# Optimization experiments

Hardware: AMD Instinct MI355X
Metric: run time of the kernel (lower is better)

## Reference

```python
import jax, jax.numpy as jnp
import numpy as np

N_TOKENS = 32768
DIM = 2048
N_EXPERTS = 64
TOP_K = 8
N_GROUP = 8
TOPK_GROUP = 4
ROUTE_SCALE = 2.5
EPS = 1e-20


def setup_inputs() -> dict:
    key = jax.random.key(0)
    k1, k2 = jax.random.split(key)
    hidden_states = jax.random.normal(k1, (N_TOKENS, DIM), dtype=jnp.float32)
    weight = jax.random.normal(k2, (N_EXPERTS, DIM), dtype=jnp.float32) * 0.02
    e_score_correction_bias = jnp.zeros((N_EXPERTS,), dtype=jnp.float32)
    return {"hidden_states": hidden_states, "weight": weight,
            "e_score_correction_bias": e_score_correction_bias}


def reference(hidden_states, weight, e_score_correction_bias):
    # router logits in fp32: [N, E]
    logits = jnp.einsum('nd,ed->ne', hidden_states.astype(jnp.float32),
                        weight.astype(jnp.float32))
    scores = jax.nn.sigmoid(logits)  # score_func == 'sigmoid'

    # --- top-k index selection (no-grad path in torch) ---
    sfc = scores + e_score_correction_bias[None, :]  # [N, E]
    per_group = N_EXPERTS // N_GROUP
    # group score = sum of top-2 scores within each group: [N, G]
    grouped = sfc.reshape(-1, N_GROUP, per_group)
    group_scores = jax.lax.top_k(grouped, 2)[0].sum(axis=-1)
    # pick top `TOPK_GROUP` groups
    _, group_idx = jax.lax.top_k(group_scores, TOPK_GROUP)  # [N, topk_group]
    n = group_scores.shape[0]
    group_mask = jnp.zeros_like(group_scores).at[
        jnp.arange(n)[:, None], group_idx].set(1.0)  # [N, G]
    score_mask = jnp.repeat(group_mask, per_group, axis=1)  # [N, E]
    masked_scores = jnp.where(score_mask > 0, sfc, 0.0)
    _, topk_indices = jax.lax.top_k(masked_scores, TOP_K)  # [N, top_k]

    # gather weights from *unbiased* scores, normalize, scale
    topk_weights = jnp.take_along_axis(scores, topk_indices, axis=1)
    denom = topk_weights.sum(axis=-1, keepdims=True) + EPS
    topk_weights = topk_weights / denom * ROUTE_SCALE
    return topk_indices, topk_weights
```

## Files before the change

### kernel.cpp

```cpp
#include <hip/hip_runtime.h>
#include <math.h>

#define NT 32768
#define DIM 2048
#define NE 64
#define RSCALE 2.5f
#define REPS 1e-20f
#define KC 64
#define NCHK (DIM / KC)
#define TOKB 32

#define WL_OFF 12288
#define BS_OFF 36864
#define ARENA 37120

typedef __attribute__((ext_vector_type(8))) short short8x;
typedef __attribute__((ext_vector_type(4))) float f32x4;
typedef __attribute__((ext_vector_type(4))) unsigned int uint4x;

#define PACKHI(odd, even) __builtin_amdgcn_perm((odd), (even), 0x07060302u)

__device__ __forceinline__ void decomp4(f32x4 x, unsigned int o[6]) {
    unsigned int u0 = __float_as_uint(x.x), u1 = __float_as_uint(x.y);
    unsigned int u2 = __float_as_uint(x.z), u3 = __float_as_uint(x.w);
    o[0] = PACKHI(u1, u0); o[1] = PACKHI(u3, u2);
    float r0 = x.x - __uint_as_float(u0 & 0xffff0000u);
    float r1 = x.y - __uint_as_float(u1 & 0xffff0000u);
    float r2 = x.z - __uint_as_float(u2 & 0xffff0000u);
    float r3 = x.w - __uint_as_float(u3 & 0xffff0000u);
    unsigned int v0 = __float_as_uint(r0), v1 = __float_as_uint(r1);
    unsigned int v2 = __float_as_uint(r2), v3 = __float_as_uint(r3);
    o[2] = PACKHI(v1, v0); o[3] = PACKHI(v3, v2);
    float s0 = r0 - __uint_as_float(v0 & 0xffff0000u);
    float s1 = r1 - __uint_as_float(v1 & 0xffff0000u);
    float s2 = r2 - __uint_as_float(v2 & 0xffff0000u);
    float s3 = r3 - __uint_as_float(v3 & 0xffff0000u);
    o[4] = PACKHI(__float_as_uint(s1), __float_as_uint(s0));
    o[5] = PACKHI(__float_as_uint(s3), __float_as_uint(s2));
}

__device__ __forceinline__ void decomp8(f32x4 a, f32x4 b,
                                        short8x* f0, short8x* f1, short8x* f2) {
    unsigned int oa[6], ob[6];
    decomp4(a, oa); decomp4(b, ob);
    uint4x t0 = {oa[0], oa[1], ob[0], ob[1]};
    uint4x t1 = {oa[2], oa[3], ob[2], ob[3]};
    uint4x t2 = {oa[4], oa[5], ob[4], ob[5]};
    *f0 = __builtin_bit_cast(short8x, t0);
    *f1 = __builtin_bit_cast(short8x, t1);
    *f2 = __builtin_bit_cast(short8x, t2);
}

#define BARRIER() do { \
    asm volatile("s_waitcnt lgkmcnt(0)" ::: "memory"); \
    __builtin_amdgcn_s_barrier(); \
    __builtin_amdgcn_sched_barrier(0); \
} while (0)

#define STAGE_ISSUE(H0, H1, W0, W1, W2, W3, KOFF) do { \
    H0 = *(const f32x4*)(hgsrc + (KOFF)); \
    H1 = *(const f32x4*)(hgsrc + (KOFF) + 4); \
    W0 = *(const f32x4*)(wgsrc + (KOFF)); \
    W1 = *(const f32x4*)(wgsrc + (KOFF) + 4); \
    W2 = *(const f32x4*)(wgsrc + (KOFF) + 8); \
    W3 = *(const f32x4*)(wgsrc + (KOFF) + 12); \
} while (0)

#define STAGE_WRITE(H0, H1, W0, W1, W2, W3) do { \
    short8x f0_, f1_, f2_; \
    decomp8(H0, H1, &f0_, &f1_, &f2_); \
    *(short8x*)(arena + 0    + hoff) = f0_; \
    *(short8x*)(arena + 4096 + hoff) = f1_; \
    *(short8x*)(arena + 8192 + hoff) = f2_; \
    decomp8(W0, W1, &f0_, &f1_, &f2_); \
    *(short8x*)(arena + WL_OFF + 0     + woff0) = f0_; \
    *(short8x*)(arena + WL_OFF + 8192  + woff0) = f1_; \
    *(short8x*)(arena + WL_OFF + 16384 + woff0) = f2_; \
    decomp8(W2, W3, &f0_, &f1_, &f2_); \
    *(short8x*)(arena + WL_OFF + 0     + woff1) = f0_; \
    *(short8x*)(arena + WL_OFF + 8192  + woff1) = f1_; \
    *(short8x*)(arena + WL_OFF + 16384 + woff1) = f2_; \
} while (0)

#define COMPUTE() do { \
    _Pragma("unroll") \
    for (int kk = 0; kk < 2; ++kk) { \
        short8x a0[2], a1[2], a2[2]; \
        _Pragma("unroll") \
        for (int tt = 0; tt < 2; ++tt) { \
            const int r_ = tt * 16 + l15; \
            const int sb = r_ * 128 + (((kk * 4 + g) ^ (r_ & 7)) << 4); \
            a0[tt] = *(const short8x*)(arena + 0    + sb); \
            a1[tt] = *(const short8x*)(arena + 4096 + sb); \
            a2[tt] = *(const short8x*)(arena + 8192 + sb); \
        } \
        const int rw = w * 16 + l15; \
        const int wb = rw * 128 + (((kk * 4 + g) ^ (rw & 7)) << 4); \
        short8x b0 = *(const short8x*)(arena + WL_OFF + 0     + wb); \
        short8x b1 = *(const short8x*)(arena + WL_OFF + 8192  + wb); \
        short8x b2 = *(const short8x*)(arena + WL_OFF + 16384 + wb); \
        _Pragma("unroll") \
        for (int tt = 0; tt < 2; ++tt) { \
            Cm[tt] = __builtin_amdgcn_mfma_f32_16x16x32_bf16(a0[tt], b0, Cm[tt], 0, 0, 0); \
            Cc[tt] = __builtin_amdgcn_mfma_f32_16x16x32_bf16(a1[tt], b0, Cc[tt], 0, 0, 0); \
            Cc[tt] = __builtin_amdgcn_mfma_f32_16x16x32_bf16(a2[tt], b0, Cc[tt], 0, 0, 0); \
            Cc[tt] = __builtin_amdgcn_mfma_f32_16x16x32_bf16(a0[tt], b1, Cc[tt], 0, 0, 0); \
            Cc[tt] = __builtin_amdgcn_mfma_f32_16x16x32_bf16(a1[tt], b1, Cc[tt], 0, 0, 0); \
            Cc[tt] = __builtin_amdgcn_mfma_f32_16x16x32_bf16(a0[tt], b2, Cc[tt], 0, 0, 0); \
        } \
    } \
} while (0)

#define DRAIN do { \
    _Pragma("unroll") \
    for (int tt = 0; tt < 2; ++tt) { \
        _Pragma("unroll") \
        for (int r = 0; r < 4; ++r) \
            md[tt][r] += (double)Cm[tt][r] + (double)Cc[tt][r]; \
        Cm[tt] = (f32x4)0.0f; Cc[tt] = (f32x4)0.0f; \
    } \
} while (0)

__global__ __launch_bounds__(256, 4) void router_kernel(
    const float* __restrict__ H,
    const float* __restrict__ W,
    const float* __restrict__ B,
    float* __restrict__ out)
{
    __shared__ __align__(16) char arena[ARENA];
    float* bsf = (float*)(arena + BS_OFF);
    float* scf = (float*)(arena);

    const int tid  = threadIdx.x;
    const int lane = tid & 63;
    const int w    = __builtin_amdgcn_readfirstlane(tid >> 6);
    const int l15  = lane & 15, g = lane >> 4;
    const size_t tb = (size_t)blockIdx.x * TOKB;

    if (tid < NE) bsf[tid] = B[tid];

    const int hrow = tid >> 3, hq = tid & 7;
    const int wrow = tid >> 2, wq = (tid & 3) << 1;
    const float* hgsrc = H + (tb + (size_t)hrow) * DIM + hq * 8;
    const float* wgsrc = W + (size_t)wrow * DIM + wq * 8;
    const int hoff  = hrow * 128 + ((hq ^ (hrow & 7)) << 4);
    const int woff0 = wrow * 128 + ((wq ^ (wrow & 7)) << 4);
    const int woff1 = wrow * 128 + (((wq + 1) ^ (wrow & 7)) << 4);

    f32x4 Cm[2], Cc[2];
    double md[2][4];
    #pragma unroll
    for (int tt = 0; tt < 2; ++tt) {
        Cm[tt] = (f32x4)0.0f; Cc[tt] = (f32x4)0.0f;
        #pragma unroll
        for (int r = 0; r < 4; ++r) md[tt][r] = 0.0;
    }

    f32x4 hA0, hA1, wA0, wA1, wA2, wA3;
    f32x4 hB0, hB1, wB0, wB1, wB2, wB3;

    STAGE_ISSUE(hA0, hA1, wA0, wA1, wA2, wA3, 0);
    STAGE_ISSUE(hB0, hB1, wB0, wB1, wB2, wB3, KC);
    STAGE_WRITE(hA0, hA1, wA0, wA1, wA2, wA3);
    BARRIER();

    for (int chb = 0; chb < NCHK; chb += 2) {
        COMPUTE();
        if (chb + 2 < NCHK) STAGE_ISSUE(hA0, hA1, wA0, wA1, wA2, wA3, (chb + 2) * KC);
        BARRIER();
        STAGE_WRITE(hB0, hB1, wB0, wB1, wB2, wB3);
        BARRIER();

        COMPUTE();
        if (chb + 3 < NCHK) STAGE_ISSUE(hB0, hB1, wB0, wB1, wB2, wB3, (chb + 3) * KC);
        if (((chb + 1) & 3) == 3) DRAIN;
        BARRIER();
        if (chb + 2 < NCHK) STAGE_WRITE(hA0, hA1, wA0, wA1, wA2, wA3);
        BARRIER();
    }

    #pragma unroll
    for (int tt = 0; tt < 2; ++tt)
        #pragma unroll
        for (int r = 0; r < 4; ++r) {
            float logit = (float)md[tt][r];
            float s = 1.0f / (1.0f + expf(-logit));
            int t = tt * 16 + g * 4 + r;
            int e = w * 16 + l15;
            scf[t * 65 + e] = s;
        }
    __syncthreads();

    if ((tid & 7) == 0) {
        const int t = tid >> 3;
        const float* sc = &scf[t * 65];
        float gs[8];
        #pragma unroll
        for (int gg = 0; gg < 8; ++gg) {
            float m1 = -1e30f, m2 = -1e30f;
            #pragma unroll
            for (int j = 0; j < 8; ++j) {
                float v = sc[gg * 8 + j] + bsf[gg * 8 + j];
                if (v > m1) { m2 = m1; m1 = v; }
                else if (v > m2) { m2 = v; }
            }
            gs[gg] = m1 + m2;
        }
        unsigned gmask = 0;
        for (int i = 0; i < 4; ++i) {
            float best = -1e30f; int bg = 0;
            for (int gg = 0; gg < 8; ++gg)
                if (!((gmask >> gg) & 1u) && gs[gg] > best) { best = gs[gg]; bg = gg; }
            gmask |= 1u << bg;
        }
        unsigned long long picked = 0ull;
        int   idxs[8];
        float wts[8];
        float wsum = 0.0f;
        for (int i = 0; i < 8; ++i) {
            float best = -1e30f; int bi = 0;
            for (int e = 0; e < 64; ++e) {
                if ((picked >> e) & 1ull) continue;
                float v = ((gmask >> (e >> 3)) & 1u) ? (sc[e] + bsf[e]) : 0.0f;
                if (v > best) { best = v; bi = e; }
            }
            picked |= 1ull << bi;
            idxs[i] = bi;
            wts[i] = sc[bi];
            wsum += sc[bi];
        }
        const float scale = RSCALE / (wsum + REPS);
        const size_t token = tb + t;
        #pragma unroll
        for (int i = 0; i < 8; ++i) {
            out[token * 8 + i] = (float)idxs[i];
            out[(size_t)NT * 8 + token * 8 + i] = wts[i] * scale;
        }
    }
}

extern "C" void kernel_launch(void* const* d_in, const int* in_sizes, int n_in,
                              void* d_out, int out_size, void* d_ws, size_t ws_size,
                              hipStream_t stream) {
    (void)in_sizes; (void)n_in; (void)out_size; (void)d_ws; (void)ws_size;
    const float* H = (const float*)d_in[0];
    const float* W = (const float*)d_in[1];
    const float* B = (const float*)d_in[2];
    float* out = (float*)d_out;
    router_kernel<<<dim3(NT / TOKB), dim3(256), 0, stream>>>(H, W, B, out);
}
```

Baseline: 148.9 us.

## Pre-split weights once and stream per-wave slices via direct global-to-LDS loads

Adds a small prep kernel that splits the router weight into three bf16 parts in a pre-swizzled global image. The main kernel then loads each wave's weight slice straight into a per-wave LDS region with global_load_lds, and keeps hidden-state chunks in registers, splitting them right before the MFMAs. This removes the block-wide barriers, the per-block weight split work and the LDS staging of activations, and it halves the K chunk size. The costs are an extra kernel launch, a hand-set vmcnt wait that must stay in step with the number of loads in flight, and redundant hidden loads, since every wave reads all 32 token rows.

New measurement: 221.3 us. +48.6%, slower.

```diff
diff --git a/kernel.cpp b/kernel.cpp
--- a/kernel.cpp
+++ b/kernel.cpp
@@ -6,17 +6,22 @@
 #define NE 64
 #define RSCALE 2.5f
 #define REPS 1e-20f
-#define KC 64
-#define NCHK (DIM / KC)
+#define KC 32
+#define NCH (DIM / KC)
 #define TOKB 32
 
-#define WL_OFF 12288
-#define BS_OFF 36864
-#define ARENA 37120
-
+#define WAVE_LDS 6144
+#define BUF_STRIDE 3072
+#define BS_OFF 24576
+#define ARENA 24832
+
+typedef const __attribute__((address_space(1))) void GV;
+typedef __attribute__((address_space(3))) void LV;
 typedef __attribute__((ext_vector_type(8))) short short8x;
 typedef __attribute__((ext_vector_type(4))) float f32x4;
 typedef __attribute__((ext_vector_type(4))) unsigned int uint4x;
+
+__device__ __align__(16) char WImg[NCH][3 * 4096];
 
 #define PACKHI(odd, even) __builtin_amdgcn_perm((odd), (even), 0x07060302u)
 
@@ -51,63 +56,59 @@
     *f2 = __builtin_bit_cast(short8x, t2);
 }
 
-#define BARRIER() do { \
-    asm volatile("s_waitcnt lgkmcnt(0)" ::: "memory"); \
-    __builtin_amdgcn_s_barrier(); \
-    __builtin_amdgcn_sched_barrier(0); \
-} while (0)
-
-#define STAGE_ISSUE(H0, H1, W0, W1, W2, W3, KOFF) do { \
-    H0 = *(const f32x4*)(hgsrc + (KOFF)); \
-    H1 = *(const f32x4*)(hgsrc + (KOFF) + 4); \
-    W0 = *(const f32x4*)(wgsrc + (KOFF)); \
-    W1 = *(const f32x4*)(wgsrc + (KOFF) + 4); \
-    W2 = *(const f32x4*)(wgsrc + (KOFF) + 8); \
-    W3 = *(const f32x4*)(wgsrc + (KOFF) + 12); \
-} while (0)
-
-#define STAGE_WRITE(H0, H1, W0, W1, W2, W3) do { \
-    short8x f0_, f1_, f2_; \
-    decomp8(H0, H1, &f0_, &f1_, &f2_); \
-    *(short8x*)(arena + 0    + hoff) = f0_; \
-    *(short8x*)(arena + 4096 + hoff) = f1_; \
-    *(short8x*)(arena + 8192 + hoff) = f2_; \
-    decomp8(W0, W1, &f0_, &f1_, &f2_); \
-    *(short8x*)(arena + WL_OFF + 0     + woff0) = f0_; \
-    *(short8x*)(arena + WL_OFF + 8192  + woff0) = f1_; \
-    *(short8x*)(arena + WL_OFF + 16384 + woff0) = f2_; \
-    decomp8(W2, W3, &f0_, &f1_, &f2_); \
-    *(short8x*)(arena + WL_OFF + 0     + woff1) = f0_; \
-    *(short8x*)(arena + WL_OFF + 8192  + woff1) = f1_; \
-    *(short8x*)(arena + WL_OFF + 16384 + woff1) = f2_; \
-} while (0)
-
-#define COMPUTE() do { \
+__global__ void prep_w_kernel(const float* __restrict__ W) {
+    const int ch = blockIdx.x;
+    const int tid = threadIdx.x;
+    const int srow = tid >> 2;
+    const int sq   = tid & 3;
+    const float* src = W + (size_t)srow * DIM + ch * KC + sq * 8;
+    f32x4 lo = *(const f32x4*)src;
+    f32x4 hi = *(const f32x4*)(src + 4);
+    short8x f0, f1, f2;
+    decomp8(lo, hi, &f0, &f1, &f2);
+    const int soff = srow * 64 + ((sq ^ ((srow >> 1) & 3)) << 4);
+    *(short8x*)&WImg[ch][0 * 4096 + soff] = f0;
+    *(short8x*)&WImg[ch][1 * 4096 + soff] = f1;
+    *(short8x*)&WImg[ch][2 * 4096 + soff] = f2;
+}
+
+#define SB __builtin_amdgcn_sched_barrier(0)
+
+#define VWAIT() do { SB; asm volatile("s_waitcnt vmcnt(7)" ::: "memory"); SB; } while (0)
+
+#define HSTAGE(R0, R1, R2, R3, CHN) do { \
+    const float* p0_ = hg0 + (CHN) * KC; \
+    const float* p1_ = hg1 + (CHN) * KC; \
+    R0 = *(const f32x4*)p0_; R1 = *(const f32x4*)(p0_ + 4); \
+    R2 = *(const f32x4*)p1_; R3 = *(const f32x4*)(p1_ + 4); \
+} while (0)
+
+#define WSTAGE(CHN, BUFB) do { \
+    const char* ws_ = WImg[(CHN)]; \
+    __builtin_amdgcn_global_load_lds((GV*)(ws_ + 0 * 4096 + wimg_off), \
+        (LV*)(warena + (BUFB) + 0 * 1024), 16, 0, 0); \
+    __builtin_amdgcn_global_load_lds((GV*)(ws_ + 1 * 4096 + wimg_off), \
+        (LV*)(warena + (BUFB) + 1 * 1024), 16, 0, 0); \
+    __builtin_amdgcn_global_load_lds((GV*)(ws_ + 2 * 4096 + wimg_off), \
+        (LV*)(warena + (BUFB) + 2 * 1024), 16, 0, 0); \
+} while (0)
+
+#define COMPUTE(BUFB, R0, R1, R2, R3) do { \
+    short8x a0[2], a1[2], a2[2]; \
+    decomp8(R0, R1, &a0[0], &a1[0], &a2[0]); \
+    decomp8(R2, R3, &a0[1], &a1[1], &a2[1]); \
+    const char* wb_ = warena + (BUFB); \
+    short8x b0 = *(const short8x*)(wb_ + 0 * 1024 + bo); \
+    short8x b1 = *(const short8x*)(wb_ + 1 * 1024 + bo); \
+    short8x b2 = *(const short8x*)(wb_ + 2 * 1024 + bo); \
     _Pragma("unroll") \
-    for (int kk = 0; kk < 2; ++kk) { \
-        short8x a0[2], a1[2], a2[2]; \
-        _Pragma("unroll") \
-        for (int tt = 0; tt < 2; ++tt) { \
-            const int r_ = tt * 16 + l15; \
-            const int sb = r_ * 128 + (((kk * 4 + g) ^ (r_ & 7)) << 4); \
-            a0[tt] = *(const short8x*)(arena + 0    + sb); \
-            a1[tt] = *(const short8x*)(arena + 4096 + sb); \
-            a2[tt] = *(const short8x*)(arena + 8192 + sb); \
-        } \
-        const int rw = w * 16 + l15; \
-        const int wb = rw * 128 + (((kk * 4 + g) ^ (rw & 7)) << 4); \
-        short8x b0 = *(const short8x*)(arena + WL_OFF + 0     + wb); \
-        short8x b1 = *(const short8x*)(arena + WL_OFF + 8192  + wb); \
-        short8x b2 = *(const short8x*)(arena + WL_OFF + 16384 + wb); \
-        _Pragma("unroll") \
-        for (int tt = 0; tt < 2; ++tt) { \
-            Cm[tt] = __builtin_amdgcn_mfma_f32_16x16x32_bf16(a0[tt], b0, Cm[tt], 0, 0, 0); \
-            Cc[tt] = __builtin_amdgcn_mfma_f32_16x16x32_bf16(a1[tt], b0, Cc[tt], 0, 0, 0); \
-            Cc[tt] = __builtin_amdgcn_mfma_f32_16x16x32_bf16(a2[tt], b0, Cc[tt], 0, 0, 0); \
-            Cc[tt] = __builtin_amdgcn_mfma_f32_16x16x32_bf16(a0[tt], b1, Cc[tt], 0, 0, 0); \
-            Cc[tt] = __builtin_amdgcn_mfma_f32_16x16x32_bf16(a1[tt], b1, Cc[tt], 0, 0, 0); \
-            Cc[tt] = __builtin_amdgcn_mfma_f32_16x16x32_bf16(a0[tt], b2, Cc[tt], 0, 0, 0); \
-        } \
+    for (int tt = 0; tt < 2; ++tt) { \
+        Cm[tt] = __builtin_amdgcn_mfma_f32_16x16x32_bf16(a0[tt], b0, Cm[tt], 0, 0, 0); \
+        Cc[tt] = __builtin_amdgcn_mfma_f32_16x16x32_bf16(a1[tt], b0, Cc[tt], 0, 0, 0); \
+        Cc[tt] = __builtin_amdgcn_mfma_f32_16x16x32_bf16(a2[tt], b0, Cc[tt], 0, 0, 0); \
+        Cc[tt] = __builtin_amdgcn_mfma_f32_16x16x32_bf16(a0[tt], b1, Cc[tt], 0, 0, 0); \
+        Cc[tt] = __builtin_amdgcn_mfma_f32_16x16x32_bf16(a1[tt], b1, Cc[tt], 0, 0, 0); \
+        Cc[tt] = __builtin_amdgcn_mfma_f32_16x16x32_bf16(a0[tt], b2, Cc[tt], 0, 0, 0); \
     } \
 } while (0)
 
@@ -123,7 +124,6 @@
 
 __global__ __launch_bounds__(256, 4) void router_kernel(
     const float* __restrict__ H,
-    const float* __restrict__ W,
     const float* __restrict__ B,
     float* __restrict__ out)
 {
@@ -137,15 +137,13 @@
     const int l15  = lane & 15, g = lane >> 4;
     const size_t tb = (size_t)blockIdx.x * TOKB;
 
-    if (tid < NE) bsf[tid] = B[tid];
-
-    const int hrow = tid >> 3, hq = tid & 7;
-    const int wrow = tid >> 2, wq = (tid & 3) << 1;
-    const float* hgsrc = H + (tb + (size_t)hrow) * DIM + hq * 8;
-    const float* wgsrc = W + (size_t)wrow * DIM + wq * 8;
-    const int hoff  = hrow * 128 + ((hq ^ (hrow & 7)) << 4);
-    const int woff0 = wrow * 128 + ((wq ^ (wrow & 7)) << 4);
-    const int woff1 = wrow * 128 + (((wq + 1) ^ (wrow & 7)) << 4);
+    float breg = (tid < NE) ? B[tid] : 0.0f;
+
+    char* warena = arena + w * WAVE_LDS;
+    const int wimg_off = w * 1024 + lane * 16;
+    const float* hg0 = H + (tb + (size_t)l15) * DIM + g * 8;
+    const float* hg1 = H + (tb + 16 + (size_t)l15) * DIM + g * 8;
+    const int bo = l15 * 64 + ((g ^ ((l15 >> 1) & 3)) << 4);
 
     f32x4 Cm[2], Cc[2];
     double md[2][4];
@@ -156,28 +154,29 @@
         for (int r = 0; r < 4; ++r) md[tt][r] = 0.0;
     }
 
-    f32x4 hA0, hA1, wA0, wA1, wA2, wA3;
-    f32x4 hB0, hB1, wB0, wB1, wB2, wB3;
-
-    STAGE_ISSUE(hA0, hA1, wA0, wA1, wA2, wA3, 0);
-    STAGE_ISSUE(hB0, hB1, wB0, wB1, wB2, wB3, KC);
-    STAGE_WRITE(hA0, hA1, wA0, wA1, wA2, wA3);
-    BARRIER();
-
-    for (int chb = 0; chb < NCHK; chb += 2) {
-        COMPUTE();
-        if (chb + 2 < NCHK) STAGE_ISSUE(hA0, hA1, wA0, wA1, wA2, wA3, (chb + 2) * KC);
-        BARRIER();
-        STAGE_WRITE(hB0, hB1, wB0, wB1, wB2, wB3);
-        BARRIER();
-
-        COMPUTE();
-        if (chb + 3 < NCHK) STAGE_ISSUE(hB0, hB1, wB0, wB1, wB2, wB3, (chb + 3) * KC);
-        if (((chb + 1) & 3) == 3) DRAIN;
-        BARRIER();
-        if (chb + 2 < NCHK) STAGE_WRITE(hA0, hA1, wA0, wA1, wA2, wA3);
-        BARRIER();
+    f32x4 hA0, hA1, hA2, hA3, hB0, hB1, hB2, hB3;
+
+    HSTAGE(hA0, hA1, hA2, hA3, 0);
+    WSTAGE(0, 0);
+
+    for (int chb = 0; chb < NCH; chb += 2) {
+        const int c1 = chb + 1;
+        const int c2 = (chb + 2 < NCH) ? chb + 2 : NCH - 1;
+
+        HSTAGE(hB0, hB1, hB2, hB3, c1);
+        WSTAGE(c1, BUF_STRIDE);
+        VWAIT();
+        COMPUTE(0, hA0, hA1, hA2, hA3);
+
+        HSTAGE(hA0, hA1, hA2, hA3, c2);
+        WSTAGE(c2, 0);
+        VWAIT();
+        COMPUTE(BUF_STRIDE, hB0, hB1, hB2, hB3);
+        if (((chb + 1) & 7) == 7) DRAIN;
     }
+
+    if (tid < NE) bsf[tid] = breg;
+    __syncthreads();
 
     #pragma unroll
     for (int tt = 0; tt < 2; ++tt)
@@ -247,5 +246,6 @@
     const float* W = (const float*)d_in[1];
     const float* B = (const float*)d_in[2];
     float* out = (float*)d_out;
-    router_kernel<<<dim3(NT / TOKB), dim3(256), 0, stream>>>(H, W, B, out);
-}
+    prep_w_kernel<<<dim3(NCH), dim3(256), 0, stream>>>(W);
+    router_kernel<<<dim3(NT / TOKB), dim3(256), 0, stream>>>(H, B, out);
+}
```
